# Performance work log

Hardware: AMD Instinct MI355X
Metric: run time of the kernel (lower is better)

The kernel has to match this reference:

```python
import jax, jax.numpy as jnp
import numpy as np

B, T, S, F_IN, F_OUT, K, L = 8, 8, 500, 32, 64, 3, 3


def setup_inputs() -> dict:
    key = jax.random.key(0)
    ks = jax.random.split(key, 10)
    x = jax.random.normal(ks[0], (B, T, S, F_IN), dtype=jnp.float32)
    Adj_t = jax.random.uniform(ks[1], (T, T), dtype=jnp.float32)
    Adj_s = jax.random.uniform(ks[2], (S, S), dtype=jnp.float32)
    # small mixing coefficients so Adj^k stays numerically tame
    s = jax.random.uniform(ks[3], (4,), dtype=jnp.float32) * 0.005
    H = jax.random.normal(ks[4], (L, K, F_OUT, F_OUT), dtype=jnp.float32) / jnp.sqrt(F_OUT)
    W1 = jax.random.normal(ks[5], (F_OUT, F_IN), dtype=jnp.float32) / jnp.sqrt(F_IN)
    b1 = jax.random.normal(ks[6], (F_OUT,), dtype=jnp.float32) * 0.01
    W2 = jax.random.normal(ks[7], (F_OUT, F_OUT), dtype=jnp.float32) / jnp.sqrt(F_OUT)
    b2 = jax.random.normal(ks[8], (F_OUT,), dtype=jnp.float32) * 0.01
    merge = jax.random.normal(ks[9], (T,), dtype=jnp.float32)
    return {"x": x, "Adj_t": Adj_t, "Adj_s": Adj_s, "s": s, "H": H,
            "W1": W1, "b1": b1, "W2": W2, "b2": b2, "merge": merge}


def reference(x, Adj_t, Adj_s, s, H, W1, b1, W2, b2, merge):
    Bx, Tx, Sx, Fin = x.shape
    N = Tx * Sx
    n_layers, Kk = H.shape[0], H.shape[1]
    I_t = jnp.eye(Tx, dtype=x.dtype)
    I_s = jnp.eye(Sx, dtype=x.dtype)
    I_st = jnp.eye(N, dtype=x.dtype)
    # mixed Kronecker product-graph adjacency, (T*S) x (T*S)
    Adj = (s[0] * I_st
           + s[1] * jnp.kron(I_t, Adj_s)
           + s[2] * jnp.kron(Adj_t, I_s)
           + s[3] * jnp.kron(Adj_t, Adj_s))
    # cache Adj^k for k = 0..K-1 (same math as per-layer matrix_power)
    powers = [I_st]
    for _ in range(1, Kk):
        powers.append(powers[-1] @ Adj)
    xf = x.reshape(Bx, N, Fin) @ W1.T + b1  # [B, N, F_out]
    for l in range(n_layers):
        acc = jnp.zeros_like(xf)
        for k in range(Kk):
            acc = acc + jnp.einsum('nm,bmf->bnf', powers[k], xf) @ H[l, k]
        xf = jnp.tanh(acc)
    xf = xf @ W2.T + b2  # [B, N, F_out]
    xo = xf.reshape(Bx, Tx, Sx, -1)  # [B, T, S, F_out]
    # transpose(3,1) -> [B,F,S,T]; matmul(merge) contracts T; transpose(2,1) -> [B,S,F]
    return jnp.einsum('btsf,t->bsf', xo, merge)
```

## Files before the change

### kernel.cpp

```cpp
#include <hip/hip_runtime.h>

#define BB 8
#define TT 8
#define SS 500
#define SP 512
#define FIN 32
#define FF 64
#define NBT 64
#define KT 1536
#define LROW_S 136
#define LROW_T 264

typedef short bf16x8 __attribute__((ext_vector_type(8)));
typedef float floatx4 __attribute__((ext_vector_type(4)));

__device__ __forceinline__ unsigned f2bf(float x) {
    unsigned u = __builtin_bit_cast(unsigned, x);
    return (u + 0x7FFFu + ((u >> 16) & 1u)) >> 16;
}
__device__ __forceinline__ float bf2f(unsigned short h) {
    unsigned u = ((unsigned)h) << 16;
    return __builtin_bit_cast(float, u);
}

__device__ __forceinline__ void ctab(int m, float s0, float s1, float s2, float s3,
                                     float& c0, float& c1, float& c2) {
    c0 = 0.f; c1 = 0.f; c2 = 0.f;
    switch (m) {
        case 0: c0 = 1.f; c1 = s0; c2 = s0 * s0; break;
        case 1: c1 = s1; c2 = 2.f * s0 * s1; break;
        case 2: c2 = s1 * s1; break;
        case 3: c1 = s2; c2 = 2.f * s0 * s2; break;
        case 4: c1 = s3; c2 = 2.f * (s0 * s3 + s1 * s2); break;
        case 5: c2 = 2.f * s1 * s3; break;
        case 6: c2 = s2 * s2; break;
        case 7: c2 = 2.f * s2 * s3; break;
        case 8: c2 = s3 * s3; break;
    }
}

__global__ __launch_bounds__(256) void setup_k(const float* __restrict__ x,
                                               const float* __restrict__ W1,
                                               const float* __restrict__ b1,
                                               const float* __restrict__ As,
                                               const float* __restrict__ At,
                                               const float* __restrict__ sc,
                                               const float* __restrict__ H,
                                               unsigned short* __restrict__ Asb,
                                               unsigned short* __restrict__ AsbT,
                                               unsigned short* __restrict__ GbigT,
                                               unsigned short* __restrict__ xfT,
                                               unsigned short* __restrict__ Abig0) {
    int tid = threadIdx.x;
    if (blockIdx.x < 512) {
        __shared__ float Xs[64][FIN + 1];
        __shared__ float Wl[FIN][FF];
        __shared__ float Ot[64][FF + 1];
        __shared__ float bl[FF];
        int bt = blockIdx.x >> 3, s0 = (blockIdx.x & 7) * 64;
        int b = bt >> 3, t = bt & 7;

        for (int i = tid; i < FIN * FF; i += 256) { int f = i >> 5, j = i & 31; Wl[j][f] = W1[i]; }
        if (tid < FF) bl[tid] = b1[tid];
        const float* xb = x + (size_t)bt * SS * FIN;
        #pragma unroll
        for (int i = 0; i < 8; ++i) {
            int lin = i * 256 + tid; int r = lin >> 5, j = lin & 31;
            int s = s0 + r;
            Xs[r][j] = (s < SS) ? xb[(size_t)s * FIN + j] : 0.f;
        }
        __syncthreads();
        int f = tid & 63, sq = tid >> 6;
        for (int i = 0; i < 16; ++i) {
            int r = sq * 16 + i;
            float acc = bl[f];
            #pragma unroll
            for (int j = 0; j < FIN; ++j) acc += Xs[r][j] * Wl[j][f];
            Ot[r][f] = (s0 + r < SS) ? acc : 0.f;
        }
        __syncthreads();
        #pragma unroll
        for (int it = 0; it < 2; ++it) {
            int idx = it * 256 + tid;
            int row = idx >> 3, c = idx & 7;
            int4 w;
            unsigned short tmp[8];
            #pragma unroll
            for (int q = 0; q < 8; ++q) tmp[q] = (unsigned short)f2bf(Ot[row][c * 8 + q]);
            w.x = tmp[0] | (tmp[1] << 16); w.y = tmp[2] | (tmp[3] << 16);
            w.z = tmp[4] | (tmp[5] << 16); w.w = tmp[6] | (tmp[7] << 16);
            *(int4*)(Abig0 + (size_t)(b * SP + s0 + row) * KT + t * 192 + c * 8) = w;
        }
        {
            int ff = tid >> 2, scol = (tid & 3) * 16;
            unsigned short tmp[16];
            #pragma unroll
            for (int i = 0; i < 16; ++i) tmp[i] = (unsigned short)f2bf(Ot[scol + i][ff]);
            unsigned short* dp = xfT + ((size_t)bt * FF + ff) * SP + s0 + scol;
            #pragma unroll
            for (int q = 0; q < 2; ++q) {
                int4 w;
                w.x = tmp[q*8+0] | (tmp[q*8+1] << 16); w.y = tmp[q*8+2] | (tmp[q*8+3] << 16);
                w.z = tmp[q*8+4] | (tmp[q*8+5] << 16); w.w = tmp[q*8+6] | (tmp[q*8+7] << 16);
                *(int4*)(dp + q * 8) = w;
            }
        }
        return;
    }
    int idx = (blockIdx.x - 512) * 256 + tid;
    if (idx < 262144) {
        int s = idx >> 9, k = idx & 511;
        Asb[idx] = (s < SS && k < SS) ? (unsigned short)f2bf(As[(size_t)s * SS + k]) : 0;
    } else if (idx < 524288) {
        int r = idx - 262144;
        int j = r >> 9, k = r & 511;
        AsbT[r] = (j < SS && k < SS) ? (unsigned short)f2bf(As[(size_t)k * SS + j]) : 0;
    } else {
        int r = idx - 524288;
        if (r < 2359296) {
            int l = r / 786432;
            int r2 = r - l * 786432;
            int t = r2 / 98304;
            int r3 = r2 - t * 98304;
            int f = r3 / 1536;
            int k = r3 - f * 1536;
            int seg = k >> 6, j = k & 63;
            int tp = seg / 3, bp = seg - tp * 3;

            float s0 = sc[0], s1 = sc[1], s2 = sc[2], s3 = sc[3];
            float w0 = (t == tp) ? 1.f : 0.f;
            float w1 = At[t * 8 + tp];
            float w2 = 0.f;
            #pragma unroll
            for (int kk = 0; kk < 8; ++kk) w2 += At[t * 8 + kk] * At[kk * 8 + tp];

            float a0, a1, a2, b0, b1, b2, d0, d1, d2;
            ctab(0 * 3 + bp, s0, s1, s2, s3, a0, a1, a2);
            ctab(1 * 3 + bp, s0, s1, s2, s3, b0, b1, b2);
            ctab(2 * 3 + bp, s0, s1, s2, s3, d0, d1, d2);
            float k0c = w0 * a0 + w1 * b0 + w2 * d0;
            float k1c = w0 * a1 + w1 * b1 + w2 * d1;
            float k2c = w0 * a2 + w1 * b2 + w2 * d2;

            float val = k0c * H[((size_t)(l * 3 + 0) * 64 + j) * 64 + f]
                      + k1c * H[((size_t)(l * 3 + 1) * 64 + j) * 64 + f]
                      + k2c * H[((size_t)(l * 3 + 2) * 64 + j) * 64 + f];
            GbigT[r] = (unsigned short)f2bf(val);
        }
    }
}

__global__ __launch_bounds__(256) void prep2_k(const unsigned short* __restrict__ Asb,
                                               const unsigned short* __restrict__ AsbT,
                                               unsigned short* __restrict__ Asqb) {
    int tid = threadIdx.x;
    int wave = tid >> 6, lane = tid & 63;
    int l16 = lane & 15, quad = lane >> 4;
    int st = blockIdx.x, ct = blockIdx.y;

    const unsigned short* ap = Asb + (size_t)(st * 16 + l16) * SP + quad * 8;
    const unsigned short* bp = AsbT + (size_t)(ct * 64 + wave * 16 + l16) * SP + quad * 8;
    floatx4 acc = {};
    #pragma unroll 4
    for (int k0 = 0; k0 < SP; k0 += 32)
        acc = __builtin_amdgcn_mfma_f32_16x16x32_bf16(*(const bf16x8*)(ap + k0),
                                                      *(const bf16x8*)(bp + k0), acc, 0, 0, 0);
    int j = ct * 64 + wave * 16 + l16;
    int i0 = st * 16 + quad * 4;
    #pragma unroll
    for (int r = 0; r < 4; ++r)
        Asqb[(size_t)(i0 + r) * SP + j] = (unsigned short)f2bf(acc[r]);
}

__global__ __launch_bounds__(256) void smm_k(const unsigned short* __restrict__ Asb,
                                             const unsigned short* __restrict__ Asqb,
                                             const unsigned short* __restrict__ xfT,
                                             unsigned short* __restrict__ Abig) {
    __shared__ unsigned short A1[64 * LROW_S];
    __shared__ unsigned short A2[64 * LROW_S];
    __shared__ unsigned short Bt[64 * LROW_S];

    int tid = threadIdx.x;
    int wave = tid >> 6, lane = tid & 63;
    int l16 = lane & 15, quad = lane >> 4;
    int m0 = blockIdx.x * 64, bt = blockIdx.y;
    int b = bt >> 3, t = bt & 7;

    const unsigned short* a1g = Asb + (size_t)m0 * SP;
    const unsigned short* a2g = Asqb + (size_t)m0 * SP;
    const unsigned short* bg  = xfT + (size_t)bt * FF * SP;

    floatx4 acc1[4] = {}, acc2[4] = {};

    for (int k0 = 0; k0 < SP; k0 += 128) {
        __syncthreads();
        #pragma unroll
        for (int it = 0; it < 4; ++it) {
            int idx = it * 256 + tid;
            int row = idx >> 4, c = idx & 15;
            int4 v1 = *(const int4*)(a1g + (size_t)row * SP + k0 + c * 8);
            int4 v2 = *(const int4*)(a2g + (size_t)row * SP + k0 + c * 8);
            int4 vb = *(const int4*)(bg  + (size_t)row * SP + k0 + c * 8);
            *(int4*)&A1[row * LROW_S + c * 8] = v1;
            *(int4*)&A2[row * LROW_S + c * 8] = v2;
            *(int4*)&Bt[row * LROW_S + c * 8] = vb;
        }
        __syncthreads();
        #pragma unroll
        for (int ks = 0; ks < 4; ++ks) {
            bf16x8 af1 = *(const bf16x8*)&A1[(wave * 16 + l16) * LROW_S + ks * 32 + quad * 8];
            bf16x8 af2 = *(const bf16x8*)&A2[(wave * 16 + l16) * LROW_S + ks * 32 + quad * 8];
            #pragma unroll
            for (int nt = 0; nt < 4; ++nt) {
                bf16x8 bf = *(const bf16x8*)&Bt[(nt * 16 + l16) * LROW_S + ks * 32 + quad * 8];
                acc1[nt] = __builtin_amdgcn_mfma_f32_16x16x32_bf16(af1, bf, acc1[nt], 0, 0, 0);
                acc2[nt] = __builtin_amdgcn_mfma_f32_16x16x32_bf16(af2, bf, acc2[nt], 0, 0, 0);
            }
        }
    }

    __syncthreads();
    #pragma unroll
    for (int nt = 0; nt < 4; ++nt)
        #pragma unroll
        for (int r = 0; r < 4; ++r) {
            A1[(wave * 16 + quad * 4 + r) * LROW_S + nt * 16 + l16] = (unsigned short)f2bf(acc1[nt][r]);
            A2[(wave * 16 + quad * 4 + r) * LROW_S + nt * 16 + l16] = (unsigned short)f2bf(acc2[nt][r]);
        }
    __syncthreads();
    int row = wave * 16 + (lane >> 2);
    int c2 = (lane & 3) * 2;
    #pragma unroll
    for (int q = 0; q < 2; ++q) {
        int c = c2 + q;
        int4 v1 = *(const int4*)&A1[row * LROW_S + c * 8];
        int4 v2 = *(const int4*)&A2[row * LROW_S + c * 8];
        size_t base = (size_t)(b * SP + m0 + row) * KT + t * 192;
        *(int4*)(Abig + base + 64 + c * 8)  = v1;
        *(int4*)(Abig + base + 128 + c * 8) = v2;
    }
}

__global__ __launch_bounds__(256) void tmix_k(const unsigned short* __restrict__ Abig,
                                              const unsigned short* __restrict__ GbigT_l,
                                              unsigned short* __restrict__ xfT_out,
                                              unsigned short* __restrict__ Abig_out,
                                              int wflag) {
    __shared__ unsigned short At_[64 * LROW_T];
    __shared__ unsigned short Bt_[64 * LROW_T];

    int tid = threadIdx.x;
    int wave = tid >> 6, lane = tid & 63;
    int l16 = lane & 15, quad = lane >> 4;
    int mi = wave & 1, ni = wave >> 1;
    int m0 = blockIdx.x * 64, t = blockIdx.y;
    int b = m0 >> 9, s0 = m0 & 511;

    const unsigned short* ag = Abig + (size_t)m0 * KT;
    const unsigned short* bg = GbigT_l + (size_t)t * FF * KT;

    floatx4 acc[2][2] = {};

    for (int kk = 0; kk < 6; ++kk) {
        __syncthreads();
        #pragma unroll
        for (int it = 0; it < 8; ++it) {
            int idx = it * 256 + tid;
            int row = idx >> 5, c = idx & 31;
            int4 va = *(const int4*)(ag + (size_t)row * KT + kk * 256 + c * 8);
            int4 vb = *(const int4*)(bg + (size_t)row * KT + kk * 256 + c * 8);
            *(int4*)&At_[row * LROW_T + c * 8] = va;
            *(int4*)&Bt_[row * LROW_T + c * 8] = vb;
        }
        __syncthreads();
        #pragma unroll
        for (int ks = 0; ks < 8; ++ks) {
            bf16x8 af[2], bf[2];
            #pragma unroll
            for (int mt = 0; mt < 2; ++mt)
                af[mt] = *(const bf16x8*)&At_[(mi * 32 + mt * 16 + l16) * LROW_T + ks * 32 + quad * 8];
            #pragma unroll
            for (int nt = 0; nt < 2; ++nt)
                bf[nt] = *(const bf16x8*)&Bt_[(ni * 32 + nt * 16 + l16) * LROW_T + ks * 32 + quad * 8];
            #pragma unroll
            for (int mt = 0; mt < 2; ++mt)
                #pragma unroll
                for (int nt = 0; nt < 2; ++nt)
                    acc[mt][nt] = __builtin_amdgcn_mfma_f32_16x16x32_bf16(af[mt], bf[nt], acc[mt][nt], 0, 0, 0);
        }
    }

    #pragma unroll
    for (int mt = 0; mt < 2; ++mt)
        #pragma unroll
        for (int nt = 0; nt < 2; ++nt)
            #pragma unroll
            for (int r = 0; r < 4; ++r) acc[mt][nt][r] = tanhf(acc[mt][nt][r]);

    int bt = b * 8 + t;

    if (wflag) {
        #pragma unroll
        for (int mt = 0; mt < 2; ++mt) {
            int sbase = s0 + mi * 32 + mt * 16 + quad * 4;
            #pragma unroll
            for (int nt = 0; nt < 2; ++nt) {
                int f = ni * 32 + nt * 16 + l16;
                int2 w;
                w.x = (int)(f2bf(acc[mt][nt][0]) | (f2bf(acc[mt][nt][1]) << 16));
                w.y = (int)(f2bf(acc[mt][nt][2]) | (f2bf(acc[mt][nt][3]) << 16));
                *(int2*)(xfT_out + ((size_t)bt * FF + f) * SP + sbase) = w;
            }
        }
    }

    __syncthreads();
    #pragma unroll
    for (int mt = 0; mt < 2; ++mt)
        #pragma unroll
        for (int nt = 0; nt < 2; ++nt)
            #pragma unroll
            for (int r = 0; r < 4; ++r)
                At_[(mi * 32 + mt * 16 + quad * 4 + r) * LROW_T + ni * 32 + nt * 16 + l16] =
                    (unsigned short)f2bf(acc[mt][nt][r]);
    __syncthreads();
    {
        int row = wave * 16 + (lane >> 2);
        int c2 = (lane & 3) * 2;
        #pragma unroll
        for (int q = 0; q < 2; ++q) {
            int c = c2 + q;
            int4 v = *(const int4*)&At_[row * LROW_T + c * 8];
            *(int4*)(Abig_out + (size_t)(m0 + row) * KT + t * 192 + c * 8) = v;
        }
    }
}

__global__ __launch_bounds__(256) void zredlin2_k(const unsigned short* __restrict__ Abig,
                                                  const float* __restrict__ W2,
                                                  const float* __restrict__ b2,
                                                  const float* __restrict__ merge,
                                                  float* __restrict__ out) {
    __shared__ float Wl[FF][FF + 1];
    __shared__ float zt[16][FF + 1];
    __shared__ float ml[TT];
    int tid = threadIdx.x;
    int b = blockIdx.y, s0 = blockIdx.x * 16;

    for (int i = tid; i < FF * FF; i += 256) { int f = i >> 6, j = i & 63; Wl[j][f] = W2[i]; }
    if (tid < TT) ml[tid] = merge[tid];
    __syncthreads();

    float m[TT];
    #pragma unroll
    for (int t = 0; t < TT; ++t) m[t] = ml[t];
    float msum = 0.f;
    #pragma unroll
    for (int t = 0; t < TT; ++t) msum += m[t];

    #pragma unroll
    for (int p = 0; p < 4; ++p) {
        int lin = p * 256 + tid;
        int sl = lin >> 6, f = lin & 63;
        int s = s0 + sl;
        float acc = 0.f;
        if (s < SS) {
            #pragma unroll
            for (int t = 0; t < TT; ++t)
                acc += m[t] * bf2f(Abig[(size_t)(b * SP + s) * KT + t * 192 + f]);
        }
        zt[sl][f] = acc;
    }
    __syncthreads();

    int f = tid & 63, sq = tid >> 6;
    #pragma unroll
    for (int i = 0; i < 4; ++i) {
        int sl = sq * 4 + i;
        int s = s0 + sl;
        if (s < SS) {
            float acc = b2[f] * msum;
            #pragma unroll
            for (int j = 0; j < FF; ++j) acc += zt[sl][j] * Wl[j][f];
            out[((size_t)b * SS + s) * FF + f] = acc;
        }
    }
}

extern "C" void kernel_launch(void* const* d_in, const int* in_sizes, int n_in,
                              void* d_out, int out_size, void* d_ws, size_t ws_size,
                              hipStream_t stream) {
    const float* x     = (const float*)d_in[0];
    const float* At    = (const float*)d_in[1];
    const float* As    = (const float*)d_in[2];
    const float* sc    = (const float*)d_in[3];
    const float* H     = (const float*)d_in[4];
    const float* W1    = (const float*)d_in[5];
    const float* b1    = (const float*)d_in[6];
    const float* W2    = (const float*)d_in[7];
    const float* b2    = (const float*)d_in[8];
    const float* merge = (const float*)d_in[9];
    float* out = (float*)d_out;

    char* ws = (char*)d_ws;
    unsigned short* Asb   = (unsigned short*)(ws + 0);
    unsigned short* AsbT  = (unsigned short*)(ws + 524288);
    unsigned short* Asqb  = (unsigned short*)(ws + 1048576);
    unsigned short* GbigT = (unsigned short*)(ws + 1572864);
    unsigned short* xfT0  = (unsigned short*)(ws + 6291456);
    unsigned short* xfT1  = (unsigned short*)(ws + 10485760);
    unsigned short* Abig0 = (unsigned short*)(ws + 14680064);
    unsigned short* Abig1 = (unsigned short*)(ws + 27262976);

    setup_k<<<11776, 256, 0, stream>>>(x, W1, b1, As, At, sc, H,
                                       Asb, AsbT, GbigT, xfT0, Abig0);
    prep2_k<<<dim3(32, 8), 256, 0, stream>>>(Asb, AsbT, Asqb);

    unsigned short* xfT_cur = xfT0;  unsigned short* xfT_nxt = xfT1;
    unsigned short* Abig_cur = Abig0; unsigned short* Abig_nxt = Abig1;
    for (int l = 0; l < 3; ++l) {
        smm_k<<<dim3(8, NBT), 256, 0, stream>>>(Asb, Asqb, xfT_cur, Abig_cur);
        tmix_k<<<dim3(64, 8), 256, 0, stream>>>(Abig_cur,
                                                GbigT + (size_t)l * 8 * FF * KT,
                                                xfT_nxt, Abig_nxt, (l < 2) ? 1 : 0);
        unsigned short* tt = xfT_cur;  xfT_cur = xfT_nxt;  xfT_nxt = tt;
        unsigned short* tb = Abig_cur; Abig_cur = Abig_nxt; Abig_nxt = tb;
    }
    zredlin2_k<<<dim3(32, 8), 256, 0, stream>>>(Abig_cur, W2, b2, merge, out);
}
```

Before: 195.2 us.

## Factor temporal mixing out of the per-layer GEMM into a small separate contraction

```diff
diff --git a/kernel.cpp b/kernel.cpp
--- a/kernel.cpp
+++ b/kernel.cpp
@@ -9,7 +9,10 @@
 #define NBT 64
 #define KT 1536
 #define LROW_S 136
-#define LROW_T 264
+#define HROW 200
+#define AROW 1544
+#define WROW 196
+#define OROW 520
 
 typedef short bf16x8 __attribute__((ext_vector_type(8)));
 typedef float floatx4 __attribute__((ext_vector_type(4)));
@@ -21,6 +24,12 @@
 __device__ __forceinline__ float bf2f(unsigned short h) {
     unsigned u = ((unsigned)h) << 16;
     return __builtin_bit_cast(float, u);
+}
+__device__ __forceinline__ float ftanh(float x) {
+    float ax = fabsf(x);
+    float e = __expf(-2.f * ax);
+    float r = (1.f - e) * __builtin_amdgcn_rcpf(1.f + e);
+    return copysignf(r, x);
 }
 
 __device__ __forceinline__ void ctab(int m, float s0, float s1, float s2, float s3,
@@ -48,7 +57,8 @@
                                                const float* __restrict__ H,
                                                unsigned short* __restrict__ Asb,
                                                unsigned short* __restrict__ AsbT,
-                                               unsigned short* __restrict__ GbigT,
+                                               unsigned short* __restrict__ HcT,
+                                               float* __restrict__ CtT,
                                                unsigned short* __restrict__ xfT,
                                                unsigned short* __restrict__ Abig0) {
     int tid = threadIdx.x;
@@ -117,35 +127,33 @@
         AsbT[r] = (j < SS && k < SS) ? (unsigned short)f2bf(As[(size_t)k * SS + j]) : 0;
     } else {
         int r = idx - 524288;
-        if (r < 2359296) {
-            int l = r / 786432;
-            int r2 = r - l * 786432;
-            int t = r2 / 98304;
-            int r3 = r2 - t * 98304;
-            int f = r3 / 1536;
-            int k = r3 - f * 1536;
-            int seg = k >> 6, j = k & 63;
-            int tp = seg / 3, bp = seg - tp * 3;
-
+        if (r < 110592) {
+            int l = r / 36864;
+            int r2 = r - l * 36864;
+            int row = r2 / 192;
+            int col = r2 - row * 192;
+            int p = row >> 6, f = row & 63;
+            int bp = col >> 6, j = col & 63;
             float s0 = sc[0], s1 = sc[1], s2 = sc[2], s3 = sc[3];
-            float w0 = (t == tp) ? 1.f : 0.f;
-            float w1 = At[t * 8 + tp];
-            float w2 = 0.f;
-            #pragma unroll
-            for (int kk = 0; kk < 8; ++kk) w2 += At[t * 8 + kk] * At[kk * 8 + tp];
-
-            float a0, a1, a2, b0, b1, b2, d0, d1, d2;
-            ctab(0 * 3 + bp, s0, s1, s2, s3, a0, a1, a2);
-            ctab(1 * 3 + bp, s0, s1, s2, s3, b0, b1, b2);
-            ctab(2 * 3 + bp, s0, s1, s2, s3, d0, d1, d2);
-            float k0c = w0 * a0 + w1 * b0 + w2 * d0;
-            float k1c = w0 * a1 + w1 * b1 + w2 * d1;
-            float k2c = w0 * a2 + w1 * b2 + w2 * d2;
-
-            float val = k0c * H[((size_t)(l * 3 + 0) * 64 + j) * 64 + f]
-                      + k1c * H[((size_t)(l * 3 + 1) * 64 + j) * 64 + f]
-                      + k2c * H[((size_t)(l * 3 + 2) * 64 + j) * 64 + f];
-            GbigT[r] = (unsigned short)f2bf(val);
+            float c0, c1, c2;
+            ctab(p * 3 + bp, s0, s1, s2, s3, c0, c1, c2);
+            float val = c0 * H[((size_t)(l * 3 + 0) * 64 + j) * 64 + f]
+                      + c1 * H[((size_t)(l * 3 + 1) * 64 + j) * 64 + f]
+                      + c2 * H[((size_t)(l * 3 + 2) * 64 + j) * 64 + f];
+            HcT[r] = (unsigned short)f2bf(val);
+        } else if (r < 110784) {
+            int i2 = r - 110592;
+            int pt = i2 >> 3, t = i2 & 7;
+            int p = pt >> 3, tp = pt & 7;
+            float val;
+            if (p == 0) val = (t == tp) ? 1.f : 0.f;
+            else if (p == 1) val = At[t * 8 + tp];
+            else {
+                val = 0.f;
+                #pragma unroll
+                for (int kk = 0; kk < 8; ++kk) val += At[t * 8 + kk] * At[kk * 8 + tp];
+            }
+            CtT[i2] = val;
         }
     }
 }
@@ -241,97 +249,126 @@
     }
 }
 
-__global__ __launch_bounds__(256) void tmix_k(const unsigned short* __restrict__ Abig,
-                                              const unsigned short* __restrict__ GbigT_l,
+__global__ __launch_bounds__(256) void hmix_k(const unsigned short* __restrict__ Abig,
+                                              const unsigned short* __restrict__ HcT_l,
+                                              const float* __restrict__ CtT,
                                               unsigned short* __restrict__ xfT_out,
                                               unsigned short* __restrict__ Abig_out,
                                               int wflag) {
-    __shared__ unsigned short At_[64 * LROW_T];
-    __shared__ unsigned short Bt_[64 * LROW_T];
+    __shared__ int4 smem4[7888];
+    __shared__ float CtS[192];
+    unsigned short* As_ = (unsigned short*)smem4;
+    unsigned short* Bs  = As_ + 16 * AROW;
+    float* Wl = (float*)smem4;
+    unsigned short* Ob = (unsigned short*)((char*)smem4 + 100352);
 
     int tid = threadIdx.x;
     int wave = tid >> 6, lane = tid & 63;
     int l16 = lane & 15, quad = lane >> 4;
-    int mi = wave & 1, ni = wave >> 1;
-    int m0 = blockIdx.x * 64, t = blockIdx.y;
-    int b = m0 >> 9, s0 = m0 & 511;
-
-    const unsigned short* ag = Abig + (size_t)m0 * KT;
-    const unsigned short* bg = GbigT_l + (size_t)t * FF * KT;
-
-    floatx4 acc[2][2] = {};
-
-    for (int kk = 0; kk < 6; ++kk) {
-        __syncthreads();
-        #pragma unroll
-        for (int it = 0; it < 8; ++it) {
-            int idx = it * 256 + tid;
-            int row = idx >> 5, c = idx & 31;
-            int4 va = *(const int4*)(ag + (size_t)row * KT + kk * 256 + c * 8);
-            int4 vb = *(const int4*)(bg + (size_t)row * KT + kk * 256 + c * 8);
-            *(int4*)&At_[row * LROW_T + c * 8] = va;
-            *(int4*)&Bt_[row * LROW_T + c * 8] = vb;
-        }
-        __syncthreads();
-        #pragma unroll
-        for (int ks = 0; ks < 8; ++ks) {
-            bf16x8 af[2], bf[2];
-            #pragma unroll
-            for (int mt = 0; mt < 2; ++mt)
-                af[mt] = *(const bf16x8*)&At_[(mi * 32 + mt * 16 + l16) * LROW_T + ks * 32 + quad * 8];
-            #pragma unroll
-            for (int nt = 0; nt < 2; ++nt)
-                bf[nt] = *(const bf16x8*)&Bt_[(ni * 32 + nt * 16 + l16) * LROW_T + ks * 32 + quad * 8];
-            #pragma unroll
-            for (int mt = 0; mt < 2; ++mt)
+    int wm = wave & 1, wn = wave >> 1;
+    int s0 = blockIdx.x * 16, b = blockIdx.y;
+
+    if (tid < 192) CtS[tid] = CtT[tid];
+
+    {
+        int ar = tid >> 4, ac = tid & 15;
+        const unsigned short* agp = Abig + (size_t)(b * SP + s0 + ar) * KT;
+        #pragma unroll
+        for (int it = 0; it < 12; ++it) {
+            int c = ac + it * 16;
+            *(int4*)&As_[ar * AROW + c * 8] = *(const int4*)(agp + c * 8);
+        }
+    }
+    {
+        int br = tid >> 3, bc = tid & 7;
+        #pragma unroll
+        for (int it = 0; it < 6; ++it) {
+            int row = it * 32 + br;
+            const unsigned short* hp = HcT_l + (size_t)row * 192;
+            #pragma unroll
+            for (int j = 0; j < 3; ++j) {
+                int c = bc + j * 8;
+                *(int4*)&Bs[row * HROW + c * 8] = *(const int4*)(hp + c * 8);
+            }
+        }
+    }
+    __syncthreads();
+
+    floatx4 acc[4][6] = {};
+    #pragma unroll
+    for (int ks = 0; ks < 6; ++ks) {
+        bf16x8 af[4], bf[6];
+        #pragma unroll
+        for (int mt = 0; mt < 4; ++mt)
+            af[mt] = *(const bf16x8*)&As_[l16 * AROW + (wm * 4 + mt) * 192 + ks * 32 + quad * 8];
+        #pragma unroll
+        for (int nt = 0; nt < 6; ++nt)
+            bf[nt] = *(const bf16x8*)&Bs[((wn * 6 + nt) * 16 + l16) * HROW + ks * 32 + quad * 8];
+        #pragma unroll
+        for (int mt = 0; mt < 4; ++mt)
+            #pragma unroll
+            for (int nt = 0; nt < 6; ++nt)
+                acc[mt][nt] = __builtin_amdgcn_mfma_f32_16x16x32_bf16(af[mt], bf[nt], acc[mt][nt], 0, 0, 0);
+    }
+
+    __syncthreads();
+    #pragma unroll
+    for (int mt = 0; mt < 4; ++mt)
+        #pragma unroll
+        for (int nt = 0; nt < 6; ++nt)
+            #pragma unroll
+            for (int r = 0; r < 4; ++r)
+                Wl[((wm * 4 + mt) * 16 + quad * 4 + r) * WROW + (wn * 6 + nt) * 16 + l16] = acc[mt][nt][r];
+    __syncthreads();
+
+    {
+        int f = tid & 63, sg = tid >> 6;
+        float o[8][4] = {};
+        #pragma unroll
+        for (int pt = 0; pt < 24; ++pt) {
+            int tp = pt & 7, p = pt >> 3;
+            float wv[4];
+            #pragma unroll
+            for (int i = 0; i < 4; ++i)
+                wv[i] = Wl[(tp * 16 + sg * 4 + i) * WROW + p * 64 + f];
+            #pragma unroll
+            for (int t = 0; t < 8; ++t) {
+                float cv = CtS[pt * 8 + t];
                 #pragma unroll
-                for (int nt = 0; nt < 2; ++nt)
-                    acc[mt][nt] = __builtin_amdgcn_mfma_f32_16x16x32_bf16(af[mt], bf[nt], acc[mt][nt], 0, 0, 0);
-        }
-    }
-
-    #pragma unroll
-    for (int mt = 0; mt < 2; ++mt)
-        #pragma unroll
-        for (int nt = 0; nt < 2; ++nt)
-            #pragma unroll
-            for (int r = 0; r < 4; ++r) acc[mt][nt][r] = tanhf(acc[mt][nt][r]);
-
-    int bt = b * 8 + t;
-
+                for (int i = 0; i < 4; ++i) o[t][i] += cv * wv[i];
+            }
+        }
+        #pragma unroll
+        for (int t = 0; t < 8; ++t)
+            #pragma unroll
+            for (int i = 0; i < 4; ++i)
+                Ob[(sg * 4 + i) * OROW + t * 64 + f] = (unsigned short)f2bf(ftanh(o[t][i]));
+    }
+    __syncthreads();
+
+    #pragma unroll
+    for (int it = 0; it < 4; ++it) {
+        int u = it * 256 + tid;
+        int sl = u >> 6, t = (u >> 3) & 7, c = u & 7;
+        int4 v = *(const int4*)&Ob[sl * OROW + t * 64 + c * 8];
+        *(int4*)(Abig_out + (size_t)(b * SP + s0 + sl) * KT + t * 192 + c * 8) = v;
+    }
     if (wflag) {
         #pragma unroll
-        for (int mt = 0; mt < 2; ++mt) {
-            int sbase = s0 + mi * 32 + mt * 16 + quad * 4;
-            #pragma unroll
-            for (int nt = 0; nt < 2; ++nt) {
-                int f = ni * 32 + nt * 16 + l16;
-                int2 w;
-                w.x = (int)(f2bf(acc[mt][nt][0]) | (f2bf(acc[mt][nt][1]) << 16));
-                w.y = (int)(f2bf(acc[mt][nt][2]) | (f2bf(acc[mt][nt][3]) << 16));
-                *(int2*)(xfT_out + ((size_t)bt * FF + f) * SP + sbase) = w;
-            }
-        }
-    }
-
-    __syncthreads();
-    #pragma unroll
-    for (int mt = 0; mt < 2; ++mt)
-        #pragma unroll
-        for (int nt = 0; nt < 2; ++nt)
-            #pragma unroll
-            for (int r = 0; r < 4; ++r)
-                At_[(mi * 32 + mt * 16 + quad * 4 + r) * LROW_T + ni * 32 + nt * 16 + l16] =
-                    (unsigned short)f2bf(acc[mt][nt][r]);
-    __syncthreads();
-    {
-        int row = wave * 16 + (lane >> 2);
-        int c2 = (lane & 3) * 2;
-        #pragma unroll
-        for (int q = 0; q < 2; ++q) {
-            int c = c2 + q;
-            int4 v = *(const int4*)&At_[row * LROW_T + c * 8];
-            *(int4*)(Abig_out + (size_t)(m0 + row) * KT + t * 192 + c * 8) = v;
+        for (int it = 0; it < 2; ++it) {
+            int u = it * 256 + tid;
+            int t = u >> 6, f = u & 63;
+            unsigned short tmp[16];
+            #pragma unroll
+            for (int sl = 0; sl < 16; ++sl) tmp[sl] = Ob[sl * OROW + t * 64 + f];
+            unsigned short* dp = xfT_out + ((size_t)(b * 8 + t) * FF + f) * SP + s0;
+            #pragma unroll
+            for (int q = 0; q < 2; ++q) {
+                int4 w;
+                w.x = tmp[q*8+0] | (tmp[q*8+1] << 16); w.y = tmp[q*8+2] | (tmp[q*8+3] << 16);
+                w.z = tmp[q*8+4] | (tmp[q*8+5] << 16); w.w = tmp[q*8+6] | (tmp[q*8+7] << 16);
+                *(int4*)(dp + q * 8) = w;
+            }
         }
     }
 }
@@ -406,22 +443,23 @@
     unsigned short* Asb   = (unsigned short*)(ws + 0);
     unsigned short* AsbT  = (unsigned short*)(ws + 524288);
     unsigned short* Asqb  = (unsigned short*)(ws + 1048576);
-    unsigned short* GbigT = (unsigned short*)(ws + 1572864);
+    unsigned short* HcT   = (unsigned short*)(ws + 1572864);
+    float*          CtT   = (float*)(ws + 1794048);
     unsigned short* xfT0  = (unsigned short*)(ws + 6291456);
     unsigned short* xfT1  = (unsigned short*)(ws + 10485760);
     unsigned short* Abig0 = (unsigned short*)(ws + 14680064);
     unsigned short* Abig1 = (unsigned short*)(ws + 27262976);
 
-    setup_k<<<11776, 256, 0, stream>>>(x, W1, b1, As, At, sc, H,
-                                       Asb, AsbT, GbigT, xfT0, Abig0);
+    setup_k<<<2993, 256, 0, stream>>>(x, W1, b1, As, At, sc, H,
+                                      Asb, AsbT, HcT, CtT, xfT0, Abig0);
     prep2_k<<<dim3(32, 8), 256, 0, stream>>>(Asb, AsbT, Asqb);
 
     unsigned short* xfT_cur = xfT0;  unsigned short* xfT_nxt = xfT1;
     unsigned short* Abig_cur = Abig0; unsigned short* Abig_nxt = Abig1;
     for (int l = 0; l < 3; ++l) {
         smm_k<<<dim3(8, NBT), 256, 0, stream>>>(Asb, Asqb, xfT_cur, Abig_cur);
-        tmix_k<<<dim3(64, 8), 256, 0, stream>>>(Abig_cur,
-                                                GbigT + (size_t)l * 8 * FF * KT,
+        hmix_k<<<dim3(32, 8), 256, 0, stream>>>(Abig_cur,
+                                                HcT + (size_t)l * 36864, CtT,
                                                 xfT_nxt, Abig_nxt, (l < 2) ? 1 : 0);
         unsigned short* tt = xfT_cur;  xfT_cur = xfT_nxt;  xfT_nxt = tt;
         unsigned short* tb = Abig_cur; Abig_cur = Abig_nxt; Abig_nxt = tb;
```

After: 165.6 us. -15.2%, faster.
